# Optimization experiments

Measured on AMD Instinct MI355X. Metric: run time of the kernel, lower is better.

## Reference

```python
import jax, jax.numpy as jnp
import numpy as np

N_NODES = 50000
N_EDGES = 800000
D = 64
N_TAPS = 3  # taps[0..3] -> 4 linear layers


def setup_inputs() -> dict:
    key = jax.random.key(0)
    k1, k2, k3, k4 = jax.random.split(key, 4)
    x = jax.random.normal(k1, (N_NODES, D), dtype=jnp.float32)
    edge_index = jax.random.randint(k2, (2, N_EDGES), 0, N_NODES, dtype=jnp.int32)
    # Glorot-ish scaled weights for the K+1 taps, bias init zeros-like but random here
    W = jax.random.normal(k3, (N_TAPS + 1, D, D), dtype=jnp.float32) / jnp.sqrt(D)
    b = jax.random.normal(k4, (N_TAPS + 1, D), dtype=jnp.float32) * 0.01
    return {"x": x, "edge_index": edge_index, "W": W, "b": b}


def reference(x, edge_index, W, b):
    # y = sum_k W_k S^k x, where S is the (sum-aggregation) graph shift:
    # out[dst] += x[src]  (PyG SimpleConv, combine_root=None, edge_attr=None)
    src, dst = edge_index[0], edge_index[1]
    # tap 0: identity shift
    y = x @ W[0].T + b[0]
    for k in range(1, N_TAPS + 1):
        # sparse graph shift: gather source features, scatter-sum to targets
        x = jax.ops.segment_sum(x[src], dst, num_segments=N_NODES)
        y = y + x @ W[k].T + b[k]
    return y
```

## Files before the change

kernel.cpp:

```cpp
#include <hip/hip_runtime.h>

#define D 64
#define NB 512
#define NBK_MAX 128
#define BCAP 10240

typedef __attribute__((ext_vector_type(8))) short bf16x8;
typedef __attribute__((ext_vector_type(4))) float f32x4;

__device__ __forceinline__ unsigned int bf16r(float f) {
    unsigned int u = __float_as_uint(f);
    return (u + 0x7fffu + ((u >> 16) & 1u)) >> 16;
}
__device__ __forceinline__ float bflo(unsigned int u) { return __uint_as_float(u << 16); }
__device__ __forceinline__ float bfhi(unsigned int u) { return __uint_as_float(u & 0xffff0000u); }

__global__ __launch_bounds__(256) void p1_kernel(
    const float* __restrict__ x, unsigned short* __restrict__ xb, int n8,
    const float* __restrict__ W, unsigned short* __restrict__ Wb, int w8,
    const int* __restrict__ src, const int* __restrict__ dst, int n_edges,
    int* __restrict__ bcursor, int* __restrict__ bpack, int nbk,
    int cgrid, int wgrid)
{
    __shared__ int lh[NBK_MAX * 8];
    __shared__ int lbase[NBK_MAX * 8];

    int tid = threadIdx.x;
    int bi  = blockIdx.x;

    if (bi < cgrid + wgrid) {
        const float* in; unsigned short* out; int t;
        if (bi < cgrid) { in = x; out = xb; t = bi * 256 + tid; if (t >= n8) return; }
        else            { in = W; out = Wb; t = (bi - cgrid) * 256 + tid; if (t >= w8) return; }
        const float4* p = reinterpret_cast<const float4*>(in) + (size_t)t * 2;
        float4 v0 = p[0], v1 = p[1];
        uint4 o;
        o.x = bf16r(v0.x) | (bf16r(v0.y) << 16);
        o.y = bf16r(v0.z) | (bf16r(v0.w) << 16);
        o.z = bf16r(v1.x) | (bf16r(v1.y) << 16);
        o.w = bf16r(v1.z) | (bf16r(v1.w) << 16);
        reinterpret_cast<uint4*>(out)[t] = o;
        return;
    }

    for (int t = tid; t < NBK_MAX * 8; t += 256) lh[t] = 0;
    __syncthreads();

    int pb = bi - cgrid - wgrid;
    int e4 = pb * 1024 + tid * 4;
    int r  = tid & 7;

    int dv[4], sv[4], bk[4], lo[4];
    bool ok[4];
    if (e4 + 4 <= n_edges) {
        int4 dd = *reinterpret_cast<const int4*>(dst + e4);
        int4 ss = *reinterpret_cast<const int4*>(src + e4);
        dv[0] = dd.x; dv[1] = dd.y; dv[2] = dd.z; dv[3] = dd.w;
        sv[0] = ss.x; sv[1] = ss.y; sv[2] = ss.z; sv[3] = ss.w;
        ok[0] = ok[1] = ok[2] = ok[3] = true;
    } else {
        #pragma unroll
        for (int j = 0; j < 4; ++j) {
            ok[j] = (e4 + j < n_edges);
            dv[j] = ok[j] ? dst[e4 + j] : 0;
            sv[j] = ok[j] ? src[e4 + j] : 0;
        }
    }
    #pragma unroll
    for (int j = 0; j < 4; ++j) {
        bk[j] = dv[j] >> 9;
        if (ok[j]) lo[j] = atomicAdd(&lh[(bk[j] << 3) | r], 1);
    }
    __syncthreads();

    if (tid < nbk) {
        int tot = 0, pbs[8];
        #pragma unroll
        for (int rr = 0; rr < 8; ++rr) { pbs[rr] = tot; tot += lh[(tid << 3) | rr]; }
        int gb = atomicAdd(&bcursor[tid], tot);
        #pragma unroll
        for (int rr = 0; rr < 8; ++rr) lbase[(tid << 3) | rr] = gb + pbs[rr];
    }
    __syncthreads();

    #pragma unroll
    for (int j = 0; j < 4; ++j) {
        if (ok[j]) {
            int pos = lbase[(bk[j] << 3) | r] + lo[j];
            bpack[bk[j] * BCAP + pos] = sv[j] | ((dv[j] & (NB - 1)) << 20);
        }
    }
}

__global__ __launch_bounds__(512) void p2_kernel(
    const int* __restrict__ bcursor, const int* __restrict__ bpack,
    int* __restrict__ rp, int* __restrict__ csr,
    int n_nodes, int n_edges, int nbk)
{
    __shared__ int sz[NBK_MAX];
    __shared__ int lh[NB];
    __shared__ int ls[NB];

    int tid = threadIdx.x;
    int bk  = blockIdx.x;

    for (int t = tid; t < NBK_MAX; t += 512) sz[t] = (t < nbk) ? bcursor[t] : 0;
    lh[tid] = 0;
    __syncthreads();
    if (tid == 0) {
        int a = 0;
        for (int i = 0; i < nbk; ++i) { int c = sz[i]; sz[i] = a; a += c; }
    }
    __syncthreads();

    int cnt      = bcursor[bk];
    int csr_base = sz[bk];
    const int* bp = bpack + (size_t)bk * BCAP;

    for (int i = tid; i < cnt; i += 512) atomicAdd(&lh[bp[i] >> 20], 1);
    __syncthreads();

    int v = lh[tid];
    ls[tid] = v;
    __syncthreads();
    for (int off = 1; off < 512; off <<= 1) {
        int t = (tid >= off) ? ls[tid - off] : 0;
        __syncthreads();
        ls[tid] += t;
        __syncthreads();
    }
    int ex = ls[tid] - v;

    int node = bk * NB + tid;
    if (node < n_nodes) rp[node] = csr_base + ex;
    if (bk == nbk - 1 && tid == 0) rp[n_nodes] = n_edges;
    __syncthreads();

    lh[tid] = ex;
    __syncthreads();
    for (int i = tid; i < cnt; i += 512) {
        int p = bp[i];
        int pos = atomicAdd(&lh[p >> 20], 1);
        csr[csr_base + pos] = p & 0xFFFFF;
    }
}

__global__ __launch_bounds__(256) void tap_kernel(
    const float* __restrict__ xin, const float* __restrict__ W,
    const float* __restrict__ b, float* __restrict__ y,
    int n_nodes, int first)
{
    __shared__ float Wt[D * (D + 1)];
    __shared__ float bs[D];
    __shared__ float xs[4][D];

    int tid = threadIdx.x;
    for (int t = tid; t < D * D; t += 256) {
        int j = t >> 6, i = t & 63;
        Wt[i * (D + 1) + j] = W[t];
    }
    if (tid < D) bs[tid] = b[tid];

    int rl = tid >> 6;
    int j  = tid & 63;
    int row = blockIdx.x * 4 + rl;
    if (row < n_nodes) xs[rl][j] = xin[(size_t)row * D + j];
    __syncthreads();

    if (row >= n_nodes) return;

    float acc = bs[j];
    #pragma unroll 8
    for (int i = 0; i < D; ++i)
        acc = fmaf(xs[rl][i], Wt[i * (D + 1) + j], acc);

    float* yp = y + (size_t)row * D + j;
    *yp = first ? acc : (*yp + acc);
}

__global__ __launch_bounds__(256) void mfma_tap_kernel(
    const unsigned short* __restrict__ X0, const unsigned short* __restrict__ X1,
    const unsigned short* __restrict__ X2, const unsigned short* __restrict__ X3,
    const unsigned short* __restrict__ Wb, const float* __restrict__ b,
    float* __restrict__ y, int n_tiles)
{
    int wv   = threadIdx.x >> 6;
    int lane = threadIdx.x & 63;
    int tile = blockIdx.x * 4 + wv;
    if (tile >= n_tiles) return;

    int col = lane & 15;
    int kg  = lane >> 4;

    f32x4 acc[4];
    #pragma unroll
    for (int jt = 0; jt < 4; ++jt) {
        int c = jt * 16 + col;
        float bias = b[c] + b[64 + c] + b[128 + c] + b[192 + c];
        acc[jt] = (f32x4){bias, bias, bias, bias};
    }

    const unsigned short* Xs[4] = {X0, X1, X2, X3};
    size_t arow = (size_t)(tile * 16 + col) * D + kg * 8;

    #pragma unroll
    for (int m = 0; m < 4; ++m) {
        const unsigned short* Xm = Xs[m];
        #pragma unroll
        for (int s = 0; s < 2; ++s) {
            bf16x8 a = *reinterpret_cast<const bf16x8*>(Xm + arow + s * 32);
            #pragma unroll
            for (int jt = 0; jt < 4; ++jt) {
                bf16x8 bb = *reinterpret_cast<const bf16x8*>(
                    Wb + m * 4096 + (jt * 16 + col) * D + s * 32 + kg * 8);
                acc[jt] = __builtin_amdgcn_mfma_f32_16x16x32_bf16(a, bb, acc[jt], 0, 0, 0);
            }
        }
    }

    #pragma unroll
    for (int jt = 0; jt < 4; ++jt) {
        #pragma unroll
        for (int r = 0; r < 4; ++r) {
            int row = kg * 4 + r;
            y[(size_t)(tile * 16 + row) * D + jt * 16 + col] = acc[jt][r];
        }
    }
}

__global__ __launch_bounds__(256) void pull_bf16_kernel(
    const unsigned short* __restrict__ xin, unsigned short* __restrict__ xout,
    const int* __restrict__ rp, const int* __restrict__ csr, int n_nodes)
{
    int tid  = threadIdx.x;
    int wid  = (blockIdx.x * 256 + tid) >> 6;
    int lane = tid & 63;
    int half = lane >> 5;
    int hl   = lane & 31;
    int hb   = half << 5;
    int g    = (lane >> 3) & 3;
    int cl   = lane & 7;
    int node = wid * 2 + half;

    int beg = 0, end = 0;
    if (node < n_nodes) { beg = rp[node]; end = rp[node + 1]; }
    int cnt  = end - beg;
    int cntO = __shfl_xor(cnt, 32);
    int maxcnt = cnt > cntO ? cnt : cntO;

    const uint4* xu = reinterpret_cast<const uint4*>(xin);
    float a0 = 0.f, a1 = 0.f, a2 = 0.f, a3 = 0.f;
    float a4 = 0.f, a5 = 0.f, a6 = 0.f, a7 = 0.f;

    for (int base = 0; base < maxcnt; base += 32) {
        int t = base + hl;
        int idx = (t < cnt) ? csr[beg + t] : 0;
        #pragma unroll
        for (int ii = 0; ii < 4; ++ii) {
            int el = 4 * ii + g;
            int s = __shfl(idx, hb + el);
            if (base + el < cnt) {
                uint4 u = xu[(size_t)s * 8 + cl];
                a0 += bflo(u.x); a1 += bfhi(u.x);
                a2 += bflo(u.y); a3 += bfhi(u.y);
                a4 += bflo(u.z); a5 += bfhi(u.z);
                a6 += bflo(u.w); a7 += bfhi(u.w);
            }
        }
        if (maxcnt - base > 16) {
            #pragma unroll
            for (int ii = 4; ii < 8; ++ii) {
                int el = 4 * ii + g;
                int s = __shfl(idx, hb + el);
                if (base + el < cnt) {
                    uint4 u = xu[(size_t)s * 8 + cl];
                    a0 += bflo(u.x); a1 += bfhi(u.x);
                    a2 += bflo(u.y); a3 += bfhi(u.y);
                    a4 += bflo(u.z); a5 += bfhi(u.z);
                    a6 += bflo(u.w); a7 += bfhi(u.w);
                }
            }
        }
    }

    a0 += __shfl_xor(a0, 8);  a1 += __shfl_xor(a1, 8);
    a2 += __shfl_xor(a2, 8);  a3 += __shfl_xor(a3, 8);
    a4 += __shfl_xor(a4, 8);  a5 += __shfl_xor(a5, 8);
    a6 += __shfl_xor(a6, 8);  a7 += __shfl_xor(a7, 8);
    a0 += __shfl_xor(a0, 16); a1 += __shfl_xor(a1, 16);
    a2 += __shfl_xor(a2, 16); a3 += __shfl_xor(a3, 16);
    a4 += __shfl_xor(a4, 16); a5 += __shfl_xor(a5, 16);
    a6 += __shfl_xor(a6, 16); a7 += __shfl_xor(a7, 16);

    if (node < n_nodes && g == 0) {
        uint4 o;
        o.x = bf16r(a0) | (bf16r(a1) << 16);
        o.y = bf16r(a2) | (bf16r(a3) << 16);
        o.z = bf16r(a4) | (bf16r(a5) << 16);
        o.w = bf16r(a6) | (bf16r(a7) << 16);
        reinterpret_cast<uint4*>(xout)[(size_t)node * 8 + cl] = o;
    }
}

__global__ __launch_bounds__(256) void scatter_kernel(
    const float* __restrict__ xin, float* __restrict__ xout,
    const int* __restrict__ src, const int* __restrict__ dst, int n_edges)
{
    int t = blockIdx.x * blockDim.x + threadIdx.x;
    int e = t >> 4;
    if (e >= n_edges) return;
    int c = (t & 15) * 4;
    int s = src[e];
    int d = dst[e];
    const float4 v = *reinterpret_cast<const float4*>(xin + (size_t)s * D + c);
    float* o = xout + (size_t)d * D + c;
    atomicAdd(o + 0, v.x);
    atomicAdd(o + 1, v.y);
    atomicAdd(o + 2, v.z);
    atomicAdd(o + 3, v.w);
}

extern "C" void kernel_launch(void* const* d_in, const int* in_sizes, int n_in,
                              void* d_out, int out_size, void* d_ws, size_t ws_size,
                              hipStream_t stream) {
    const float* x  = (const float*)d_in[0];
    const int*   ei = (const int*)d_in[1];
    const float* W  = (const float*)d_in[2];
    const float* b  = (const float*)d_in[3];
    float* y = (float*)d_out;

    int n_nodes = in_sizes[0] / D;
    int n_edges = in_sizes[1] / 2;
    const int* src = ei;
    const int* dst = ei + n_edges;

    int nbk = (n_nodes + NB - 1) / NB;

    size_t bufElems = (size_t)n_nodes * D;
    unsigned short* xb = (unsigned short*)d_ws;
    unsigned short* Ab = xb + bufElems;
    unsigned short* Bb = Ab + bufElems;
    unsigned short* Cb = Bb + bufElems;
    unsigned short* Wb = Cb + bufElems;
    int* bcursor = (int*)(Wb + 4 * D * D);
    int* bpack   = bcursor + NBK_MAX;
    int* rp      = bpack + (size_t)nbk * BCAP;
    int* csr     = rp + n_nodes + 64;

    size_t needed = (char*)(csr + n_edges) - (char*)d_ws;

    dim3 tb(256);
    dim3 tg((n_nodes + 3) / 4);
    int n8     = (int)(bufElems / 8);
    int cgrid  = (n8 + 255) / 256;
    int w8     = 4 * D * D / 8;
    int wgrid  = (w8 + 255) / 256;
    int eb     = (n_edges + 1023) / 1024;
    int pgrid  = ((n_nodes + 1) / 2 + 3) / 4;
    int n_tiles = (n_nodes + 15) / 16;
    int mgrid  = (n_tiles + 3) / 4;

    if (needed <= ws_size && (n_nodes & 15) == 0 && nbk <= NBK_MAX) {
        hipMemsetAsync(bcursor, 0, NBK_MAX * sizeof(int), stream);
        p1_kernel<<<cgrid + wgrid + eb, tb, 0, stream>>>(
            x, xb, n8, W, Wb, w8, src, dst, n_edges, bcursor, bpack, nbk,
            cgrid, wgrid);
        p2_kernel<<<nbk, 512, 0, stream>>>(bcursor, bpack, rp, csr,
                                           n_nodes, n_edges, nbk);

        pull_bf16_kernel<<<pgrid, tb, 0, stream>>>(xb, Ab, rp, csr, n_nodes);
        pull_bf16_kernel<<<pgrid, tb, 0, stream>>>(Ab, Bb, rp, csr, n_nodes);
        pull_bf16_kernel<<<pgrid, tb, 0, stream>>>(Bb, Cb, rp, csr, n_nodes);

        mfma_tap_kernel<<<mgrid, tb, 0, stream>>>(xb, Ab, Bb, Cb, Wb, b, y, n_tiles);
    } else {
        float* A = (float*)d_ws;
        float* B = A + bufElems;
        size_t bufBytes = bufElems * sizeof(float);
        int sgrid = (n_edges * 16 + 255) / 256;
        hipMemsetAsync(A, 0, bufBytes, stream);
        hipMemsetAsync(B, 0, bufBytes, stream);
        tap_kernel<<<tg, tb, 0, stream>>>(x, W, b, y, n_nodes, 1);
        scatter_kernel<<<sgrid, tb, 0, stream>>>(x, A, src, dst, n_edges);
        tap_kernel<<<tg, tb, 0, stream>>>(A, W + D * D, b + D, y, n_nodes, 0);
        scatter_kernel<<<sgrid, tb, 0, stream>>>(A, B, src, dst, n_edges);
        hipMemsetAsync(A, 0, bufBytes, stream);
        tap_kernel<<<tg, tb, 0, stream>>>(B, W + 2 * D * D, b + 2 * D, y, n_nodes, 0);
        scatter_kernel<<<sgrid, tb, 0, stream>>>(B, A, src, dst, n_edges);
        tap_kernel<<<tg, tb, 0, stream>>>(A, W + 3 * D * D, b + 3 * D, y, n_nodes, 0);
    }
}
```

Measured before the change: 117.9 us.

## Stage bucketed edges in LDS to coalesce bpack writes, 4096 edges per block

The edge-bucketing pass now handles 4096 edges per block instead of 1024. It counts per-bucket histograms, prefix-scans the bucket sizes, and writes packed entries into a shared-memory staging array ordered by bucket. Each bucket's slice is then copied contiguously to global bpack, replacing scattered per-edge global stores with coalesced runs. In exchange, src/dst are read twice, a 128-entry scan adds several barriers, the block uses more LDS (which may lower occupancy), and there are fewer blocks.

```diff
diff --git a/kernel.cpp b/kernel.cpp
--- a/kernel.cpp
+++ b/kernel.cpp
@@ -4,6 +4,7 @@
 #define NB 512
 #define NBK_MAX 128
 #define BCAP 10240
+#define EPB 4096
 
 typedef __attribute__((ext_vector_type(8))) short bf16x8;
 typedef __attribute__((ext_vector_type(4))) float f32x4;
@@ -23,7 +24,11 @@
     int cgrid, int wgrid)
 {
     __shared__ int lh[NBK_MAX * 8];
-    __shared__ int lbase[NBK_MAX * 8];
+    __shared__ int lrb[NBK_MAX * 8];
+    __shared__ int lsb[NBK_MAX];
+    __shared__ int lgb[NBK_MAX];
+    __shared__ int ltot[NBK_MAX];
+    __shared__ int stage[EPB];
 
     int tid = threadIdx.x;
     int bi  = blockIdx.x;
@@ -47,48 +52,83 @@
     __syncthreads();
 
     int pb = bi - cgrid - wgrid;
-    int e4 = pb * 1024 + tid * 4;
-    int r  = tid & 7;
-
-    int dv[4], sv[4], bk[4], lo[4];
-    bool ok[4];
-    if (e4 + 4 <= n_edges) {
-        int4 dd = *reinterpret_cast<const int4*>(dst + e4);
-        int4 ss = *reinterpret_cast<const int4*>(src + e4);
-        dv[0] = dd.x; dv[1] = dd.y; dv[2] = dd.z; dv[3] = dd.w;
-        sv[0] = ss.x; sv[1] = ss.y; sv[2] = ss.z; sv[3] = ss.w;
-        ok[0] = ok[1] = ok[2] = ok[3] = true;
-    } else {
-        #pragma unroll
-        for (int j = 0; j < 4; ++j) {
-            ok[j] = (e4 + j < n_edges);
-            dv[j] = ok[j] ? dst[e4 + j] : 0;
-            sv[j] = ok[j] ? src[e4 + j] : 0;
-        }
-    }
+    int ebase = pb * EPB;
+    int r = tid & 7;
+    int lo[16];
+
     #pragma unroll
-    for (int j = 0; j < 4; ++j) {
-        bk[j] = dv[j] >> 9;
-        if (ok[j]) lo[j] = atomicAdd(&lh[(bk[j] << 3) | r], 1);
-    }
-    __syncthreads();
-
-    if (tid < nbk) {
+    for (int k = 0; k < 4; ++k) {
+        int e4 = ebase + (tid + k * 256) * 4;
+        if (e4 + 4 <= n_edges) {
+            int4 dd = *reinterpret_cast<const int4*>(dst + e4);
+            lo[k * 4 + 0] = atomicAdd(&lh[((dd.x >> 9) << 3) | r], 1);
+            lo[k * 4 + 1] = atomicAdd(&lh[((dd.y >> 9) << 3) | r], 1);
+            lo[k * 4 + 2] = atomicAdd(&lh[((dd.z >> 9) << 3) | r], 1);
+            lo[k * 4 + 3] = atomicAdd(&lh[((dd.w >> 9) << 3) | r], 1);
+        } else {
+            #pragma unroll
+            for (int j = 0; j < 4; ++j)
+                if (e4 + j < n_edges)
+                    lo[k * 4 + j] = atomicAdd(&lh[((dst[e4 + j] >> 9) << 3) | r], 1);
+        }
+    }
+    __syncthreads();
+
+    if (tid < NBK_MAX) {
         int tot = 0, pbs[8];
         #pragma unroll
         for (int rr = 0; rr < 8; ++rr) { pbs[rr] = tot; tot += lh[(tid << 3) | rr]; }
-        int gb = atomicAdd(&bcursor[tid], tot);
         #pragma unroll
-        for (int rr = 0; rr < 8; ++rr) lbase[(tid << 3) | rr] = gb + pbs[rr];
-    }
-    __syncthreads();
+        for (int rr = 0; rr < 8; ++rr) lrb[(tid << 3) | rr] = pbs[rr];
+        ltot[tid] = tot;
+        lsb[tid] = tot;
+        if (tid < nbk && tot > 0) lgb[tid] = atomicAdd(&bcursor[tid], tot);
+    }
+    __syncthreads();
+    for (int off = 1; off < NBK_MAX; off <<= 1) {
+        int v = 0;
+        if (tid < NBK_MAX && tid >= off) v = lsb[tid - off];
+        __syncthreads();
+        if (tid < NBK_MAX) lsb[tid] += v;
+        __syncthreads();
+    }
 
     #pragma unroll
-    for (int j = 0; j < 4; ++j) {
-        if (ok[j]) {
-            int pos = lbase[(bk[j] << 3) | r] + lo[j];
-            bpack[bk[j] * BCAP + pos] = sv[j] | ((dv[j] & (NB - 1)) << 20);
-        }
+    for (int k = 0; k < 4; ++k) {
+        int e4 = ebase + (tid + k * 256) * 4;
+        if (e4 + 4 <= n_edges) {
+            int4 dd = *reinterpret_cast<const int4*>(dst + e4);
+            int4 ss = *reinterpret_cast<const int4*>(src + e4);
+            int bks[4] = {dd.x >> 9, dd.y >> 9, dd.z >> 9, dd.w >> 9};
+            int dvs[4] = {dd.x, dd.y, dd.z, dd.w};
+            int svs[4] = {ss.x, ss.y, ss.z, ss.w};
+            #pragma unroll
+            for (int j = 0; j < 4; ++j) {
+                int bk = bks[j];
+                int pos = (lsb[bk] - ltot[bk]) + lrb[(bk << 3) | r] + lo[k * 4 + j];
+                stage[pos] = svs[j] | ((dvs[j] & (NB - 1)) << 20);
+            }
+        } else {
+            #pragma unroll
+            for (int j = 0; j < 4; ++j) {
+                if (e4 + j < n_edges) {
+                    int dv = dst[e4 + j];
+                    int bk = dv >> 9;
+                    int pos = (lsb[bk] - ltot[bk]) + lrb[(bk << 3) | r] + lo[k * 4 + j];
+                    stage[pos] = src[e4 + j] | ((dv & (NB - 1)) << 20);
+                }
+            }
+        }
+    }
+    __syncthreads();
+
+    for (int bk = 0; bk < nbk; ++bk) {
+        int len = ltot[bk];
+        if (len == 0) continue;
+        int sb = lsb[bk] - len;
+        int gb = lgb[bk];
+        int* dstp = bpack + (size_t)bk * BCAP + gb;
+        for (int i = tid; i < len; i += 256) dstp[i] = stage[sb + i];
     }
 }
 
@@ -355,7 +395,7 @@
     int cgrid  = (n8 + 255) / 256;
     int w8     = 4 * D * D / 8;
     int wgrid  = (w8 + 255) / 256;
-    int eb     = (n_edges + 1023) / 1024;
+    int eb     = (n_edges + EPB - 1) / EPB;
     int pgrid  = ((n_nodes + 1) / 2 + 3) / 4;
     int n_tiles = (n_nodes + 15) / 16;
     int mgrid  = (n_tiles + 3) / 4;
```

After: 127.6 us. 8.3% more time.
